# Kernel optimization log

Measured on AMD Instinct MI355X. Metric: run time of the kernel, lower is better.

Reference implementation:

```python
import jax, jax.numpy as jnp
import numpy as np

EPS = 1e-5  # torch InstanceNorm2d default
C = 512

def setup_inputs() -> dict:
    key = jax.random.key(0)
    ks = jax.random.split(key, 9)
    x = jax.random.normal(ks[0], (4, C, 64, 64), dtype=jnp.float32)
    s = 0.05
    wq = jax.random.normal(ks[1], (C, C), dtype=jnp.float32) * s
    wk = jax.random.normal(ks[2], (C, C), dtype=jnp.float32) * s
    wv = jax.random.normal(ks[3], (C, C), dtype=jnp.float32) * s
    wp = jax.random.normal(ks[4], (C, C), dtype=jnp.float32) * s
    bq = jax.random.normal(ks[5], (C,), dtype=jnp.float32) * s
    bk = jax.random.normal(ks[6], (C,), dtype=jnp.float32) * s
    bv = jax.random.normal(ks[7], (C,), dtype=jnp.float32) * s
    bp = jax.random.normal(ks[8], (C,), dtype=jnp.float32) * s
    return {"x": x, "wq": wq, "bq": bq, "wk": wk, "bk": bk,
            "wv": wv, "bv": bv, "wp": wp, "bp": bp}

def _conv1x1(h, w, b):
    # 1x1 conv == per-pixel channel mixing: (b,c,h,w) x (o,c) -> (b,o,h,w)
    return jnp.einsum('bchw,oc->bohw', h, w) + b[None, :, None, None]

def reference(x, wq, bq, wk, bk, wv, bv, wp, bp):
    b, c, h, w = x.shape
    # InstanceNorm2d (affine=False): normalize each (b,c) plane over spatial dims
    mu = jnp.mean(x, axis=(2, 3), keepdims=True)
    var = jnp.mean(jnp.square(x - mu), axis=(2, 3), keepdims=True)
    hn = (x - mu) * jax.lax.rsqrt(var + EPS)
    q = _conv1x1(hn, wq, bq).reshape(b, c, h * w)
    k = _conv1x1(hn, wk, bk).reshape(b, c, h * w)
    v = _conv1x1(hn, wv, bv).reshape(b, c, h * w)
    # attn[b,i,j] = <q[:, i], k[:, j]> / sqrt(c), softmax over keys j
    attn = jnp.einsum('bci,bcj->bij', q, k) / jnp.sqrt(jnp.asarray(c, x.dtype))
    attn = jax.nn.softmax(attn, axis=2)
    # out[b,c,i] = sum_j v[b,c,j] * attn[b,i,j]
    o = jnp.einsum('bcj,bij->bci', v, attn).reshape(b, c, h, w)
    return x + _conv1x1(o, wp, bp)
```

## Files before the change

### kernel.cpp

```cpp
#include <hip/hip_runtime.h>
#include <hip/hip_bf16.h>

typedef short bf16x8 __attribute__((ext_vector_type(8)));
typedef float f32x4 __attribute__((ext_vector_type(4)));

#define CCH 512
#define NPIX 4096
#define NB 4

__device__ inline unsigned short f2bf(float f) {
  union { __hip_bfloat16 h; unsigned short u; } cv;
  cv.h = __float2bfloat16(f);
  return cv.u;
}

#define GLD16(gp, lp) __builtin_amdgcn_global_load_lds( \
    (const __attribute__((address_space(1))) unsigned int*)(gp), \
    (__attribute__((address_space(3))) unsigned int*)(lp), 16, 0, 0)

__global__ __launch_bounds__(256) void cast_weights_k(
    const float* __restrict__ w0, const float* __restrict__ w1,
    const float* __restrict__ w2, const float* __restrict__ w3,
    unsigned short* __restrict__ out) {
  int z = blockIdx.y;
  const float* src = (z == 0) ? w0 : (z == 1) ? w1 : (z == 2) ? w2 : w3;
  long i = (long)blockIdx.x * 256 + threadIdx.x;
  out[(long)z * CCH * CCH + i] = f2bf(src[i]);
}

__global__ __launch_bounds__(256) void bias_concat_k(
    const float* __restrict__ bq, const float* __restrict__ bk,
    float* __restrict__ bqk) {
  int i = blockIdx.x * 256 + threadIdx.x;
  bqk[i] = (i < CCH) ? bq[i] : bk[i - CCH];
}

__global__ __launch_bounds__(256) void zero_l_k(float* __restrict__ lsum) {
  int i = (blockIdx.x * 256 + threadIdx.x) * 4;
  *(float4*)(lsum + i) = make_float4(0.f, 0.f, 0.f, 0.f);
}

__global__ __launch_bounds__(256) void stats_k(const float* __restrict__ x,
                                               float* __restrict__ stats) {
  long plane = blockIdx.x;
  const float4* p = (const float4*)(x + plane * NPIX);
  int t = threadIdx.x;
  float s = 0.f, q = 0.f;
  for (int c = 0; c < 4; c++) {
    float4 v = p[c * 256 + t];
    s += v.x + v.y + v.z + v.w;
    q += v.x * v.x + v.y * v.y + v.z * v.z + v.w * v.w;
  }
  for (int off = 32; off; off >>= 1) { s += __shfl_xor(s, off); q += __shfl_xor(q, off); }
  __shared__ float rs[4], rq[4];
  int w = t >> 6;
  if ((t & 63) == 0) { rs[w] = s; rq[w] = q; }
  __syncthreads();
  if (t == 0) {
    s = rs[0] + rs[1] + rs[2] + rs[3];
    q = rq[0] + rq[1] + rq[2] + rq[3];
    float mu = s * (1.f / NPIX);
    float var = q * (1.f / NPIX) - mu * mu;
    stats[2 * plane] = mu;
    stats[2 * plane + 1] = rsqrtf(var + 1e-5f);
  }
}

__global__ __launch_bounds__(256) void norm_t_k(const float* __restrict__ x,
                                                const float* __restrict__ stats,
                                                unsigned short* __restrict__ hnT) {
  int b = blockIdx.z;
  int c0 = blockIdx.y * 32, i0 = blockIdx.x * 32;
  __shared__ float tile[32][33];
  int t = threadIdx.x;
  int il = t & 31, cl = t >> 5;
  for (int r = 0; r < 4; r++) {
    int c = c0 + cl + r * 8;
    long pl = (long)b * CCH + c;
    float mu = stats[2 * pl], rsg = stats[2 * pl + 1];
    tile[cl + r * 8][il] = (x[pl * NPIX + i0 + il] - mu) * rsg;
  }
  __syncthreads();
  for (int r = 0; r < 4; r++) {
    int i = i0 + cl + r * 8;
    hnT[((long)b * NPIX + i) * CCH + c0 + il] = f2bf(tile[il][cl + r * 8]);
  }
}

#define SH(sl, ha, h, kt) do {                                               \
    const unsigned short* g_ = ((ha) ? gB : gA) + (long)(kt) * 64 +          \
                               (long)(2 * (h)) * 65536;                      \
    char* l_ = (char*)LDSu + (sl) * 65536 + (ha) * 32768 + (2 * (h)) * 8192  \
               + t * 16;                                                     \
    GLD16(g_, l_);                                                           \
    GLD16(g_ + 65536, l_ + 8192);                                            \
  } while (0)

#define READ_A(sl, half) do {                                                \
    const unsigned short* sa_ = LDSu + (sl) * 32768;                         \
    _Pragma("unroll") for (int mm = 0; mm < 4; mm++) {                       \
      int row = ((half) * 4 + mm) * 32 + wr * 16 + fr;                       \
      a_[mm][0] = *(const bf16x8*)(sa_ + row * 64 + o0_);                    \
      a_[mm][1] = *(const bf16x8*)(sa_ + row * 64 + o1_);                    \
    }                                                                        \
  } while (0)

#define READ_B(sl, half, dst) do {                                           \
    const unsigned short* sb_ = LDSu + (sl) * 32768 + 16384;                 \
    _Pragma("unroll") for (int nn = 0; nn < 2; nn++) {                       \
      int row = ((half) * 2 + nn) * 64 + wc * 16 + fr;                       \
      dst[nn][0] = *(const bf16x8*)(sb_ + row * 64 + o0_);                   \
      dst[nn][1] = *(const bf16x8*)(sb_ + row * 64 + o1_);                   \
    }                                                                        \
  } while (0)

#define MF(qm, qn, bb)                                                       \
    _Pragma("unroll") for (int mm = 0; mm < 4; mm++)                         \
      _Pragma("unroll") for (int nn = 0; nn < 2; nn++) {                     \
        acc[(qm) * 4 + mm][(qn) * 2 + nn] =                                  \
            __builtin_amdgcn_mfma_f32_16x16x32_bf16(                         \
                a_[mm][0], bb[nn][0], acc[(qm) * 4 + mm][(qn) * 2 + nn],     \
                0, 0, 0);                                                    \
        acc[(qm) * 4 + mm][(qn) * 2 + nn] =                                  \
            __builtin_amdgcn_mfma_f32_16x16x32_bf16(                         \
                a_[mm][1], bb[nn][1], acc[(qm) * 4 + mm][(qn) * 2 + nn],     \
                0, 0, 0);                                                    \
      }

#define PHASE(WN, SSTMT, RSTMT, MSTMT) do {                                  \
    if ((WN) == 4) asm volatile("s_waitcnt vmcnt(4)" ::: "memory");          \
    else if ((WN) == 2) asm volatile("s_waitcnt vmcnt(2)" ::: "memory");     \
    else if ((WN) == 0) asm volatile("s_waitcnt vmcnt(0)" ::: "memory");     \
    __builtin_amdgcn_s_barrier();                                            \
    __builtin_amdgcn_sched_barrier(0);                                       \
    SSTMT;                                                                   \
    RSTMT;                                                                   \
    asm volatile("s_waitcnt lgkmcnt(0)" ::: "memory");                       \
    __builtin_amdgcn_sched_barrier(0);                                       \
    __builtin_amdgcn_s_setprio(1);                                           \
    MSTMT;                                                                   \
    __builtin_amdgcn_s_setprio(0);                                           \
    __builtin_amdgcn_sched_barrier(0);                                       \
    __builtin_amdgcn_s_barrier();                                            \
  } while (0)

#define GROUP(sl, ktn)                                                       \
    PHASE(4, SH(sl ^ 1, 0, 0, ktn),                                         \
          { READ_A(sl, 0); READ_B(sl, 0, b0_); }, MF(0, 0, b0_));            \
    PHASE(2, SH(sl ^ 1, 1, 0, ktn), READ_B(sl, 1, b1_), MF(0, 1, b1_));      \
    PHASE(-1, SH(sl ^ 1, 0, 1, ktn), READ_A(sl, 1), MF(1, 1, b1_));          \
    PHASE(-1, SH(sl ^ 1, 1, 1, ktn), (void)0, MF(1, 0, b0_))

#define GROUP_TAIL(sl)                                                       \
    PHASE(4, (void)0, { READ_A(sl, 0); READ_B(sl, 0, b0_); }, MF(0, 0, b0_));\
    PHASE(0, (void)0, READ_B(sl, 1, b1_), MF(0, 1, b1_));                    \
    PHASE(-1, (void)0, READ_A(sl, 1), MF(1, 1, b1_));                        \
    PHASE(-1, (void)0, (void)0, MF(1, 0, b0_))

__global__ __launch_bounds__(512, 2) void gemm8p_s_k(
    const unsigned short* __restrict__ A,
    const unsigned short* __restrict__ B,
    unsigned short* __restrict__ C,
    float* __restrict__ lsum, float scale) {
  const int z = blockIdx.z;
  const long SLAB2 = (long)NPIX * 1024;
  const long SLABP = (long)NPIX * NPIX;
  A += z * SLAB2;
  B += z * SLAB2;
  const int m0 = blockIdx.y * 256, n0 = blockIdx.x * 256;
  const int t = threadIdx.x;
  const int lane = t & 63, w = t >> 6;
  const int wr = w >> 2, wc = w & 3;
  const int fr = lane & 15, fq = lane >> 4;
  const int chx = fr & 7;
  const int o0_ = (fq ^ chx) * 8, o1_ = ((fq + 4) ^ chx) * 8;

  __shared__ __align__(16) unsigned short LDSu[2 * 32768];

  f32x4 acc[8][4] = {};
  bf16x8 a_[4][2], b0_[2][2], b1_[2][2];

  const int srow = t >> 3;
  const int scol = ((t & 7) ^ (srow & 7)) * 8;
  const unsigned short* gA = A + (long)(m0 + srow) * 1024 + scol;
  const unsigned short* gB = B + (long)(n0 + srow) * 1024 + scol;

  SH(0, 0, 0, 0); SH(0, 1, 0, 0); SH(0, 0, 1, 0); SH(0, 1, 1, 0);

  GROUP(0, 1); GROUP(1, 2);
  GROUP(0, 3); GROUP(1, 4);
  GROUP(0, 5); GROUP(1, 6);
  GROUP(0, 7);
  GROUP_TAIL(1);

  float rsum[8][4];
  for (int i = 0; i < 8; i++)
    for (int r = 0; r < 4; r++) rsum[i][r] = 0.f;
  for (int i = 0; i < 8; i++) {
    int mg = m0 + i * 32 + wr * 16 + fq * 4;
    for (int j = 0; j < 4; j++) {
      int ng = n0 + j * 64 + wc * 16 + fr;
      for (int r = 0; r < 4; r++) {
        float v = exp2f(acc[i][j][r] * scale);
        rsum[i][r] += v;
        C[z * SLABP + (long)(mg + r) * 4096 + ng] = f2bf(v);
      }
    }
  }
  for (int i = 0; i < 8; i++)
    for (int r = 0; r < 4; r++) {
      float s = rsum[i][r];
      s += __shfl_xor(s, 1);
      s += __shfl_xor(s, 2);
      s += __shfl_xor(s, 4);
      s += __shfl_xor(s, 8);
      if (fr == 0)
        atomicAdd(&lsum[z * NPIX + m0 + i * 32 + wr * 16 + fq * 4 + r], s);
    }
}
#undef SH
#undef READ_A
#undef READ_B
#undef MF
#undef PHASE
#undef GROUP
#undef GROUP_TAIL

template <int XCDX, int OUTF32, int BIASM, bool RESID, bool SCALE, bool EXPSUM, bool ROWSCALE>
__global__ __launch_bounds__(256) void gemm_bt_k(
    const unsigned short* __restrict__ A, const unsigned short* __restrict__ B,
    void* __restrict__ Cv, const float* __restrict__ bias,
    const float* __restrict__ resid, float* __restrict__ lsum,
    int K, int lda, int ldb, int ldc,
    long sA, long sB, long sC, float scale) {
  int z = blockIdx.z;
  A += z * sA;
  B += z * sB;

  int bx = blockIdx.x, by = blockIdx.y;
  if (XCDX > 0) {
    int s = blockIdx.x + gridDim.x * blockIdx.y;
    int xcd = s & 7, idx = s >> 3;
    int rw = gridDim.x / XCDX;
    int rh = (gridDim.y * XCDX) >> 3;
    int rx0 = (xcd % XCDX) * rw, ry0 = (xcd / XCDX) * rh;
    bx = rx0 + idx % rw;
    by = ry0 + idx / rw;
  }
  const int n0 = bx * 128, m0 = by * 128;

  const int t = threadIdx.x;
  const int lane = t & 63, w = t >> 6;
  const int wr = w >> 1, wc = w & 1;

  __shared__ __align__(16) unsigned short As[128 * 64];
  __shared__ __align__(16) unsigned short Bs[128 * 64];

  f32x4 acc[4][4] = {};

  const int srow = t >> 3;
  const int scol = (((t & 7) ^ (srow & 7)) * 8);
  const unsigned short* ga = A + (long)(m0 + srow) * lda + scol;
  const unsigned short* gb = B + (long)(n0 + srow) * ldb + scol;
  char* lA = (char*)As + t * 16;
  char* lB = (char*)Bs + t * 16;
  const long stpa = (long)32 * lda;
  const long stpb = (long)32 * ldb;

  const int fr = lane & 15, fq = lane >> 4;
  const int chx = fr & 7;
  const unsigned short* rA = As + (wr * 64 + fr) * 64;
  const unsigned short* rB = Bs + (wc * 64 + fr) * 64;

  const int nkt = K >> 6;
  for (int kt = 0; kt < nkt; kt++) {
    const unsigned short* gak = ga + (long)kt * 64;
    const unsigned short* gbk = gb + (long)kt * 64;
    GLD16(gak, lA);
    GLD16(gak + stpa, lA + 4096);
    GLD16(gak + 2 * stpa, lA + 8192);
    GLD16(gak + 3 * stpa, lA + 12288);
    GLD16(gbk, lB);
    GLD16(gbk + stpb, lB + 4096);
    GLD16(gbk + 2 * stpb, lB + 8192);
    GLD16(gbk + 3 * stpb, lB + 12288);
    __syncthreads();
    for (int kk = 0; kk < 2; kk++) {
      const int offA = ((fq + kk * 4) ^ chx) * 8;
      bf16x8 af[4], bfr[4];
      for (int i = 0; i < 4; i++) af[i] = *(const bf16x8*)(rA + i * 1024 + offA);
      for (int i = 0; i < 4; i++) bfr[i] = *(const bf16x8*)(rB + i * 1024 + offA);
      for (int i = 0; i < 4; i++)
        for (int j = 0; j < 4; j++)
          acc[i][j] = __builtin_amdgcn_mfma_f32_16x16x32_bf16(af[i], bfr[j], acc[i][j], 0, 0, 0);
    }
    __syncthreads();
  }

  if (OUTF32) {
    float* Cf = (float*)Cv;
    for (int i = 0; i < 4; i++) {
      int mg = m0 + wr * 64 + i * 16 + fq * 4;
      for (int j = 0; j < 4; j++) {
        int ng = n0 + wc * 64 + j * 16 + fr;
        for (int r = 0; r < 4; r++) {
          float v = acc[i][j][r];
          if (SCALE) v *= scale;
          int m = mg + r;
          if (BIASM == 1) v += bias[m];
          else if (BIASM == 2) v += bias[ng];
          long off = z * sC + (long)m * ldc + ng;
          if (RESID) v += resid[off];
          Cf[off] = v;
        }
      }
    }
  } else {
    float linv[4][4];
    if (ROWSCALE) {
      for (int i = 0; i < 4; i++)
        for (int r = 0; r < 4; r++)
          linv[i][r] = 1.f / lsum[z * NPIX + m0 + wr * 64 + i * 16 + fq * 4 + r];
    }
    float rsum[4][4];
    if (EXPSUM) {
      for (int i = 0; i < 4; i++)
        for (int r = 0; r < 4; r++) rsum[i][r] = 0.f;
    }
    unsigned short* Cb = (unsigned short*)Cv;
    for (int i = 0; i < 4; i++) {
      int mg = m0 + wr * 64 + i * 16 + fq * 4;
      for (int j = 0; j < 4; j++) {
        int ng = n0 + wc * 64 + j * 16 + fr;
        for (int r = 0; r < 4; r++) {
          float v = acc[i][j][r];
          if (SCALE) v *= scale;
          if (BIASM == 1) v += bias[mg + r];
          else if (BIASM == 2) v += bias[ng];
          if (EXPSUM) { v = exp2f(v); rsum[i][r] += v; }
          if (ROWSCALE) v *= linv[i][r];
          Cb[z * sC + (long)(mg + r) * ldc + ng] = f2bf(v);
        }
      }
    }
    if (EXPSUM) {
      for (int i = 0; i < 4; i++)
        for (int r = 0; r < 4; r++) {
          float s = rsum[i][r];
          s += __shfl_xor(s, 1);
          s += __shfl_xor(s, 2);
          s += __shfl_xor(s, 4);
          s += __shfl_xor(s, 8);
          if (fr == 0)
            atomicAdd(&lsum[z * NPIX + m0 + wr * 64 + i * 16 + fq * 4 + r], s);
        }
    }
  }
}

extern "C" void kernel_launch(void* const* d_in, const int* in_sizes, int n_in,
                              void* d_out, int out_size, void* d_ws, size_t ws_size,
                              hipStream_t stream) {
  const float* x  = (const float*)d_in[0];
  const float* wq = (const float*)d_in[1];
  const float* bq = (const float*)d_in[2];
  const float* wk = (const float*)d_in[3];
  const float* bk = (const float*)d_in[4];
  const float* wv = (const float*)d_in[5];
  const float* bv = (const float*)d_in[6];
  const float* wp = (const float*)d_in[7];
  const float* bp = (const float*)d_in[8];

  char* ws = (char*)d_ws;
  const long SLAB = (long)NPIX * CCH;
  const long SLAB2 = (long)NPIX * 1024;
  const long SLABP = (long)NPIX * NPIX;

  float* stats = (float*)ws;
  float* bqk = (float*)(ws + (32l << 10));
  float* lsum = (float*)(ws + (64l << 10));
  unsigned short* wbf = (unsigned short*)(ws + (192l << 10));
  unsigned short* hnT = (unsigned short*)(ws + (192l << 10) + (1l << 21));
  unsigned short* QKt = hnT + 4 * SLAB;
  unsigned short* V   = QKt + 4 * SLAB2;
  unsigned short* Ot  = V + 4 * SLAB;
  unsigned short* S4  = Ot + 4 * SLAB;

  unsigned short* wv_bf = wbf + 2 * 262144;
  unsigned short* wp_bf = wbf + 3 * 262144;

  cast_weights_k<<<dim3(1024, 4, 1), 256, 0, stream>>>(wq, wk, wv, wp, wbf);
  bias_concat_k<<<dim3(4, 1, 1), 256, 0, stream>>>(bq, bk, bqk);
  zero_l_k<<<dim3(16, 1, 1), 256, 0, stream>>>(lsum);
  stats_k<<<dim3(NB * CCH, 1, 1), 256, 0, stream>>>(x, stats);
  norm_t_k<<<dim3(128, 16, 4), 256, 0, stream>>>(x, stats, hnT);

  gemm_bt_k<1, 0, 2, false, false, false, false><<<dim3(8, 32, 4), 256, 0, stream>>>(
      hnT, wbf, QKt, bqk, nullptr, nullptr, 512, 512, 512, 1024, SLAB, 0, SLAB2, 1.f);
  gemm_bt_k<2, 0, 1, false, false, false, false><<<dim3(32, 4, 4), 256, 0, stream>>>(
      wv_bf, hnT, V, bv, nullptr, nullptr, 512, 512, 512, 4096, 0, SLAB, SLAB, 1.f);

  const float isc2 = 0.06375871387551278f;
  gemm8p_s_k<<<dim3(16, 16, 4), 512, 0, stream>>>(QKt, QKt + 512, S4, lsum, isc2);
  gemm_bt_k<1, 0, 0, false, false, false, true><<<dim3(4, 32, 4), 256, 0, stream>>>(
      S4, V, Ot, nullptr, nullptr, lsum, 4096, 4096, 4096, 512, SLABP, SLAB, SLAB, 1.f);
  gemm_bt_k<2, 1, 1, true, false, false, false><<<dim3(32, 4, 4), 256, 0, stream>>>(
      wp_bf, Ot, d_out, bp, x, nullptr, 512, 512, 512, 4096, 0, SLAB, SLAB, 1.f);
}
```

Baseline: 297.6 us.

## Deepen QK^T GEMM prefetch to two k-tiles ahead with in-place slot refill

The score GEMM kernel now prefetches two k-tiles into both LDS slots before the main loop. Each slot is refilled in place after its sub-tiles have been read into registers, which replaces the previous one-tile-ahead double buffering. The vmcnt waits and the barrier move to after the LDS reads, so global loads have a full k-group of MFMA work to hide behind. The risk is a write-after-read hazard if LDS regions are overwritten before all waves finish reading them, and the relaxed wait points change when data is guaranteed to have arrived.

Measured after the change: 294.0 us. Within noise of the previous version (-1.2%).

```diff
diff --git a/kernel.cpp b/kernel.cpp
--- a/kernel.cpp
+++ b/kernel.cpp
@@ -127,14 +127,12 @@
                 0, 0, 0);                                                    \
       }
 
-#define PHASE(WN, SSTMT, RSTMT, MSTMT) do {                                  \
-    if ((WN) == 4) asm volatile("s_waitcnt vmcnt(4)" ::: "memory");          \
-    else if ((WN) == 2) asm volatile("s_waitcnt vmcnt(2)" ::: "memory");     \
-    else if ((WN) == 0) asm volatile("s_waitcnt vmcnt(0)" ::: "memory");     \
-    __builtin_amdgcn_s_barrier();                                            \
-    __builtin_amdgcn_sched_barrier(0);                                       \
+#define PHASE(VN, SSTMT, RSTMT, MSTMT) do {                                  \
     SSTMT;                                                                   \
     RSTMT;                                                                   \
+    if ((VN) == 8) asm volatile("s_waitcnt vmcnt(8)" ::: "memory");          \
+    else if ((VN) == 0) asm volatile("s_waitcnt vmcnt(0)" ::: "memory");     \
+    __builtin_amdgcn_s_barrier();                                            \
     asm volatile("s_waitcnt lgkmcnt(0)" ::: "memory");                       \
     __builtin_amdgcn_sched_barrier(0);                                       \
     __builtin_amdgcn_s_setprio(1);                                           \
@@ -144,18 +142,18 @@
     __builtin_amdgcn_s_barrier();                                            \
   } while (0)
 
-#define GROUP(sl, ktn)                                                       \
-    PHASE(4, SH(sl ^ 1, 0, 0, ktn),                                         \
-          { READ_A(sl, 0); READ_B(sl, 0, b0_); }, MF(0, 0, b0_));            \
-    PHASE(2, SH(sl ^ 1, 1, 0, ktn), READ_B(sl, 1, b1_), MF(0, 1, b1_));      \
-    PHASE(-1, SH(sl ^ 1, 0, 1, ktn), READ_A(sl, 1), MF(1, 1, b1_));          \
-    PHASE(-1, SH(sl ^ 1, 1, 1, ktn), (void)0, MF(1, 0, b0_))
-
-#define GROUP_TAIL(sl)                                                       \
-    PHASE(4, (void)0, { READ_A(sl, 0); READ_B(sl, 0, b0_); }, MF(0, 0, b0_));\
-    PHASE(0, (void)0, READ_B(sl, 1, b1_), MF(0, 1, b1_));                    \
+#define GROUP_S(sl, tn)                                                      \
+    PHASE(-1, (void)0, { READ_A(sl, 0); READ_B(sl, 0, b0_); }, MF(0, 0, b0_)); \
+    PHASE(-1, { SH(sl, 0, 0, tn); SH(sl, 1, 0, tn); },                       \
+          READ_B(sl, 1, b1_), MF(0, 1, b1_));                                \
+    PHASE(-1, SH(sl, 1, 1, tn), READ_A(sl, 1), MF(1, 1, b1_));               \
+    PHASE(8, SH(sl, 0, 1, tn), (void)0, MF(1, 0, b0_))
+
+#define GROUP_N(sl, VN3)                                                     \
+    PHASE(-1, (void)0, { READ_A(sl, 0); READ_B(sl, 0, b0_); }, MF(0, 0, b0_)); \
+    PHASE(-1, (void)0, READ_B(sl, 1, b1_), MF(0, 1, b1_));                   \
     PHASE(-1, (void)0, READ_A(sl, 1), MF(1, 1, b1_));                        \
-    PHASE(-1, (void)0, (void)0, MF(1, 0, b0_))
+    PHASE(VN3, (void)0, (void)0, MF(1, 0, b0_))
 
 __global__ __launch_bounds__(512, 2) void gemm8p_s_k(
     const unsigned short* __restrict__ A,
@@ -186,12 +184,15 @@
   const unsigned short* gB = B + (long)(n0 + srow) * 1024 + scol;
 
   SH(0, 0, 0, 0); SH(0, 1, 0, 0); SH(0, 0, 1, 0); SH(0, 1, 1, 0);
-
-  GROUP(0, 1); GROUP(1, 2);
-  GROUP(0, 3); GROUP(1, 4);
-  GROUP(0, 5); GROUP(1, 6);
-  GROUP(0, 7);
-  GROUP_TAIL(1);
+  SH(1, 0, 0, 1); SH(1, 1, 0, 1); SH(1, 0, 1, 1); SH(1, 1, 1, 1);
+  asm volatile("s_waitcnt vmcnt(8)" ::: "memory");
+  __builtin_amdgcn_s_barrier();
+
+  GROUP_S(0, 2); GROUP_S(1, 3);
+  GROUP_S(0, 4); GROUP_S(1, 5);
+  GROUP_S(0, 6); GROUP_S(1, 7);
+  GROUP_N(0, 0);
+  GROUP_N(1, -1);
 
   float rsum[8][4];
   for (int i = 0; i < 8; i++)
@@ -223,8 +224,8 @@
 #undef READ_B
 #undef MF
 #undef PHASE
-#undef GROUP
-#undef GROUP_TAIL
+#undef GROUP_S
+#undef GROUP_N
 
 template <int XCDX, int OUTF32, int BIASM, bool RESID, bool SCALE, bool EXPSUM, bool ROWSCALE>
 __global__ __launch_bounds__(256) void gemm_bt_k(
```
